# Kernel tuning notes

Measured on AMD Instinct MI355X. Metric: run time of the kernel, lower is better.

## Reference

```python
import math
import jax, jax.numpy as jnp
import numpy as np

S, B, H = 512, 64, 1024

def setup_inputs() -> dict:
    key = jax.random.key(0)
    ks = jax.random.split(key, 7)
    hidden = jax.random.normal(ks[0], (1, B, H), dtype=jnp.float32)
    encoder_outputs = jax.random.normal(ks[1], (S, B, H), dtype=jnp.float32)
    pe = jax.random.normal(ks[2], (B, S), dtype=jnp.float32)
    seq_mask = jax.random.bernoulli(ks[3], 0.1, (B, S))
    # nn.Linear(2H, H): weight (H, 2H), bias (H); nn.Linear(H, 1, bias=False): weight (1, H)
    Wa = jax.random.normal(ks[4], (H, 2 * H), dtype=jnp.float32) * (1.0 / math.sqrt(2 * H))
    ba = jax.random.normal(ks[5], (H,), dtype=jnp.float32) * 0.01
    Ws = jax.random.normal(ks[6], (1, H), dtype=jnp.float32) * (1.0 / math.sqrt(H))
    return {"hidden": hidden, "encoder_outputs": encoder_outputs, "pe": pe,
            "seq_mask": seq_mask, "Wa": Wa, "ba": ba, "Ws": Ws}

def reference(hidden, encoder_outputs, pe, seq_mask, Wa, ba, Ws):
    max_len, bsz, hdim = encoder_outputs.shape
    factor = 1.0 / math.sqrt(hdim)
    scale = factor * math.log(max_len)
    # repeat hidden along seq dim, concat on feature dim -> (S, B, 2H)
    h_rep = jnp.broadcast_to(hidden, (max_len, bsz, hdim))
    energy_in = jnp.concatenate([h_rep, encoder_outputs], axis=2)  # (S, B, 2H)
    e = jax.nn.relu(jnp.einsum('sbf,hf->sbh', energy_in, Wa) + ba)  # (S, B, H)
    attn = scale * jnp.einsum('sbh,oh->sbo', e, Ws)[..., 0]          # (S, B)
    attn = attn.T + pe                                               # (B, S)
    attn = jnp.where(seq_mask, jnp.float32(-1e12), attn)
    attn = jax.nn.softmax(attn, axis=1)
    return attn[:, None, :]  # (B, 1, S)
```

## Files before the change

### kernel.cpp

```cpp
#include <hip/hip_runtime.h>
#include <hip/hip_bf16.h>

#define S_LEN 512
#define BSZ 64
#define HDIM 1024
#define H2 2048

typedef float f32x4 __attribute__((ext_vector_type(4)));
typedef short short8 __attribute__((ext_vector_type(8)));
typedef __bf16 bf16x8 __attribute__((ext_vector_type(8)));

__device__ __forceinline__ unsigned short f2bf(float x) {
    union { float f; unsigned u; } v; v.f = x;
    unsigned r = (v.u + 0x7FFFu + ((v.u >> 16) & 1u)) >> 16;
    return (unsigned short)r;
}

__global__ __launch_bounds__(256) void k_zero(float* __restrict__ p) {
    p[blockIdx.x * 256 + threadIdx.x] = 0.f;
}

__global__ __launch_bounds__(256) void k_e1(const float* __restrict__ hidden,
                                            const float* __restrict__ Wa,
                                            const float* __restrict__ ba,
                                            float* __restrict__ e1) {
    __shared__ __align__(16) float hsh[HDIM];
    int b = blockIdx.x >> 2;
    int h = ((blockIdx.x & 3) << 8) + threadIdx.x;
    for (int i = threadIdx.x; i < HDIM; i += 256) hsh[i] = hidden[b * HDIM + i];
    __syncthreads();
    const float* wr = Wa + (size_t)h * H2;
    float acc = 0.f;
#pragma unroll 8
    for (int k = 0; k < HDIM; k += 4) {
        f32x4 w = *(const f32x4*)(wr + k);
        f32x4 hh = *(const f32x4*)(hsh + k);
        acc += w[0] * hh[0] + w[1] * hh[1] + w[2] * hh[2] + w[3] * hh[3];
    }
    e1[b * HDIM + h] = acc + ba[h];
}

__global__ __launch_bounds__(256) void k_packB(const float* __restrict__ Wa,
                                               unsigned short* __restrict__ wsB) {
    int ci = blockIdx.x * 256 + threadIdx.x;
    int tile = ci >> 9;
    int wi = ci & 511;
    int row = wi >> 2;
    int slot = wi & 3;
    int nt = tile >> 5, kt = tile & 31;
    int n = nt * 128 + row;
    int kk = kt * 32 + ((slot ^ ((row >> 1) & 3)) << 3);
    const float* src = Wa + (size_t)n * H2 + HDIM + kk;
    f32x4 a = *(const f32x4*)src;
    f32x4 b = *(const f32x4*)(src + 4);
    short8 o;
    o[0] = (short)f2bf(a[0]); o[1] = (short)f2bf(a[1]);
    o[2] = (short)f2bf(a[2]); o[3] = (short)f2bf(a[3]);
    o[4] = (short)f2bf(b[0]); o[5] = (short)f2bf(b[1]);
    o[6] = (short)f2bf(b[2]); o[7] = (short)f2bf(b[3]);
    *(short8*)(wsB + (size_t)ci * 8) = o;
}

__global__ __launch_bounds__(256) void k_main(const float* __restrict__ enc,
                                              const unsigned short* __restrict__ wsB,
                                              const float* __restrict__ e1,
                                              const float* __restrict__ Ws,
                                              float* __restrict__ logits) {
    __shared__ __align__(16) unsigned short As[4096];
    __shared__ __align__(16) unsigned short Bs[4096];

    int i = blockIdx.x;
    int mt = ((i >> 6) << 3) | (i & 7);
    int nt = (i >> 3) & 7;
    int r0 = mt * 128;
    int n0 = nt * 128;

    int tid = threadIdx.x;
    int lane = tid & 63, wid = tid >> 6;
    int wr = wid >> 1, wc = wid & 1;
    int c = lane & 15, g = lane >> 4;

    f32x4 acc[4][4] = {};

    for (int k0 = 0; k0 < HDIM; k0 += 32) {
        const unsigned short* bsrc = wsB + ((size_t)(nt * 32 + (k0 >> 5)) << 12);
        char* lbase = (char*)Bs + wid * 1024;
        __builtin_amdgcn_global_load_lds(
            (const __attribute__((address_space(1))) void*)(bsrc + (size_t)tid * 8),
            (__attribute__((address_space(3))) void*)lbase, 16, 0, 0);
        __builtin_amdgcn_global_load_lds(
            (const __attribute__((address_space(1))) void*)(bsrc + (size_t)(tid + 256) * 8),
            (__attribute__((address_space(3))) void*)(lbase + 4096), 16, 0, 0);

#pragma unroll
        for (int it = 0; it < 2; ++it) {
            int row = (it << 6) + (tid >> 2);
            int slot = tid & 3;
            int kk = k0 + ((slot ^ ((row >> 1) & 3)) << 3);
            const float* src = enc + (size_t)(r0 + row) * HDIM + kk;
            f32x4 a = *(const f32x4*)src;
            f32x4 b = *(const f32x4*)(src + 4);
            short8 o;
            o[0] = (short)f2bf(a[0]); o[1] = (short)f2bf(a[1]);
            o[2] = (short)f2bf(a[2]); o[3] = (short)f2bf(a[3]);
            o[4] = (short)f2bf(b[0]); o[5] = (short)f2bf(b[1]);
            o[6] = (short)f2bf(b[2]); o[7] = (short)f2bf(b[3]);
            *(short8*)((char*)As + row * 64 + slot * 16) = o;
        }
        __syncthreads();

        bf16x8 af[4], bfr[4];
#pragma unroll
        for (int m = 0; m < 4; ++m) {
            int row = wr * 64 + m * 16 + c;
            int slot = g ^ ((row >> 1) & 3);
            af[m] = *(const bf16x8*)((const char*)As + row * 64 + slot * 16);
        }
#pragma unroll
        for (int n = 0; n < 4; ++n) {
            int rowb = wc * 64 + n * 16 + c;
            int slot = g ^ ((rowb >> 1) & 3);
            bfr[n] = *(const bf16x8*)((const char*)Bs + rowb * 64 + slot * 16);
        }
#pragma unroll
        for (int m = 0; m < 4; ++m)
#pragma unroll
            for (int n = 0; n < 4; ++n)
                acc[m][n] = __builtin_amdgcn_mfma_f32_16x16x32_bf16(af[m], bfr[n], acc[m][n], 0, 0, 0);
        __syncthreads();
    }

    float wsv[4];
#pragma unroll
    for (int n = 0; n < 4; ++n) wsv[n] = Ws[n0 + wc * 64 + n * 16 + c];

#pragma unroll
    for (int m = 0; m < 4; ++m) {
#pragma unroll
        for (int j = 0; j < 4; ++j) {
            int rl = wr * 64 + m * 16 + g * 4 + j;
            int r = r0 + rl;
            int b = r & 63, sidx = r >> 6;
            const float* e1b = e1 + b * HDIM + n0 + wc * 64;
            float p = 0.f;
#pragma unroll
            for (int n = 0; n < 4; ++n) {
                float v = acc[m][n][j] + e1b[n * 16 + c];
                v = fmaxf(v, 0.f);
                p += v * wsv[n];
            }
            p += __shfl_xor(p, 1);
            p += __shfl_xor(p, 2);
            p += __shfl_xor(p, 4);
            p += __shfl_xor(p, 8);
            if (c == 0) atomicAdd(&logits[b * S_LEN + sidx], p);
        }
    }
}

__global__ __launch_bounds__(512) void k_softmax(float* __restrict__ out,
                                                 const float* __restrict__ pe,
                                                 const int* __restrict__ mask,
                                                 float scale) {
    __shared__ float red[8];
    int b = blockIdx.x, s = threadIdx.x;
    int idx = (b << 9) + s;
    float acc = out[idx];
    float logit = (mask[idx] != 0) ? -1e12f : (scale * acc + pe[idx]);
    float m = logit;
#pragma unroll
    for (int o = 32; o >= 1; o >>= 1) m = fmaxf(m, __shfl_xor(m, o));
    if ((s & 63) == 0) red[s >> 6] = m;
    __syncthreads();
    float m2 = red[0];
#pragma unroll
    for (int i2 = 1; i2 < 8; ++i2) m2 = fmaxf(m2, red[i2]);
    float e = expf(logit - m2);
    float t = e;
#pragma unroll
    for (int o = 32; o >= 1; o >>= 1) t += __shfl_xor(t, o);
    __syncthreads();
    if ((s & 63) == 0) red[s >> 6] = t;
    __syncthreads();
    float tot = 0.f;
#pragma unroll
    for (int i2 = 0; i2 < 8; ++i2) tot += red[i2];
    out[idx] = e / tot;
}

extern "C" void kernel_launch(void* const* d_in, const int* in_sizes, int n_in,
                              void* d_out, int out_size, void* d_ws, size_t ws_size,
                              hipStream_t stream) {
    const float* hidden = (const float*)d_in[0];
    const float* enc    = (const float*)d_in[1];
    const float* pe     = (const float*)d_in[2];
    const int*   mask   = (const int*)d_in[3];
    const float* Wa     = (const float*)d_in[4];
    const float* ba     = (const float*)d_in[5];
    const float* Ws     = (const float*)d_in[6];
    float* out = (float*)d_out;

    float* e1 = (float*)d_ws;
    unsigned short* wsB = (unsigned short*)((char*)d_ws + 262144);

    const float scale = 0.19494764453248462f;

    k_zero<<<128, 256, 0, stream>>>(out);
    k_e1<<<256, 256, 0, stream>>>(hidden, Wa, ba, e1);
    k_packB<<<512, 256, 0, stream>>>(Wa, wsB);
    k_main<<<2048, 256, 0, stream>>>(enc, wsB, e1, Ws, out);
    k_softmax<<<64, 512, 0, stream>>>(out, pe, mask, scale);
}
```

Before: 393.3 us.

## Pre-pack encoder outputs to bf16 tiles and load both GEMM operands via LDS DMA

Adds a separate pass that converts the fp32 encoder outputs into swizzled bf16 tiles, so the main GEMM can stream both A and B directly into LDS with global_load_lds instead of converting fp32 in every block. The aim is to stop each N-tile block from re-reading and re-converting fp32 A eight times. The cost is an extra kernel and 64MB of workspace traffic, and the fallback path is used when the workspace is too small. k_e1 is also rewritten to use one wavefront per output with a shuffle reduction, and bf16 conversion now uses native casts.

```diff
diff --git a/kernel.cpp b/kernel.cpp
--- a/kernel.cpp
+++ b/kernel.cpp
@@ -10,12 +10,6 @@
 typedef short short8 __attribute__((ext_vector_type(8)));
 typedef __bf16 bf16x8 __attribute__((ext_vector_type(8)));
 
-__device__ __forceinline__ unsigned short f2bf(float x) {
-    union { float f; unsigned u; } v; v.f = x;
-    unsigned r = (v.u + 0x7FFFu + ((v.u >> 16) & 1u)) >> 16;
-    return (unsigned short)r;
-}
-
 __global__ __launch_bounds__(256) void k_zero(float* __restrict__ p) {
     p[blockIdx.x * 256 + threadIdx.x] = 0.f;
 }
@@ -24,20 +18,21 @@
                                             const float* __restrict__ Wa,
                                             const float* __restrict__ ba,
                                             float* __restrict__ e1) {
-    __shared__ __align__(16) float hsh[HDIM];
-    int b = blockIdx.x >> 2;
-    int h = ((blockIdx.x & 3) << 8) + threadIdx.x;
-    for (int i = threadIdx.x; i < HDIM; i += 256) hsh[i] = hidden[b * HDIM + i];
-    __syncthreads();
+    int wg = blockIdx.x * 4 + (threadIdx.x >> 6);
+    int lane = threadIdx.x & 63;
+    int b = wg >> 10, h = wg & 1023;
+    const float* hr = hidden + b * HDIM;
     const float* wr = Wa + (size_t)h * H2;
     float acc = 0.f;
-#pragma unroll 8
-    for (int k = 0; k < HDIM; k += 4) {
-        f32x4 w = *(const f32x4*)(wr + k);
-        f32x4 hh = *(const f32x4*)(hsh + k);
-        acc += w[0] * hh[0] + w[1] * hh[1] + w[2] * hh[2] + w[3] * hh[3];
-    }
-    e1[b * HDIM + h] = acc + ba[h];
+#pragma unroll
+    for (int j = 0; j < 4; ++j) {
+        f32x4 hv = *(const f32x4*)(hr + j * 256 + lane * 4);
+        f32x4 wv = *(const f32x4*)(wr + j * 256 + lane * 4);
+        acc += hv[0] * wv[0] + hv[1] * wv[1] + hv[2] * wv[2] + hv[3] * wv[3];
+    }
+#pragma unroll
+    for (int o = 32; o >= 1; o >>= 1) acc += __shfl_xor(acc, o);
+    if (lane == 0) e1[wg] = acc + ba[h];
 }
 
 __global__ __launch_bounds__(256) void k_packB(const float* __restrict__ Wa,
@@ -53,19 +48,35 @@
     const float* src = Wa + (size_t)n * H2 + HDIM + kk;
     f32x4 a = *(const f32x4*)src;
     f32x4 b = *(const f32x4*)(src + 4);
-    short8 o;
-    o[0] = (short)f2bf(a[0]); o[1] = (short)f2bf(a[1]);
-    o[2] = (short)f2bf(a[2]); o[3] = (short)f2bf(a[3]);
-    o[4] = (short)f2bf(b[0]); o[5] = (short)f2bf(b[1]);
-    o[6] = (short)f2bf(b[2]); o[7] = (short)f2bf(b[3]);
-    *(short8*)(wsB + (size_t)ci * 8) = o;
-}
-
-__global__ __launch_bounds__(256) void k_main(const float* __restrict__ enc,
-                                              const unsigned short* __restrict__ wsB,
-                                              const float* __restrict__ e1,
-                                              const float* __restrict__ Ws,
-                                              float* __restrict__ logits) {
+    bf16x8 o;
+    o[0] = (__bf16)a[0]; o[1] = (__bf16)a[1]; o[2] = (__bf16)a[2]; o[3] = (__bf16)a[3];
+    o[4] = (__bf16)b[0]; o[5] = (__bf16)b[1]; o[6] = (__bf16)b[2]; o[7] = (__bf16)b[3];
+    *(bf16x8*)(wsB + (size_t)ci * 8) = o;
+}
+
+__global__ __launch_bounds__(256) void k_packA(const float* __restrict__ enc,
+                                               unsigned short* __restrict__ wsA) {
+    int ci = blockIdx.x * 256 + threadIdx.x;
+    const float* src = enc + (size_t)ci * 8;
+    f32x4 a = *(const f32x4*)src;
+    f32x4 b = *(const f32x4*)(src + 4);
+    int row_g = ci >> 7;
+    int cchunk = ci & 127;
+    int kt = cchunk >> 2, slot_src = cchunk & 3;
+    int mt = row_g >> 7, row = row_g & 127;
+    int slot = slot_src ^ ((row >> 1) & 3);
+    size_t dst = ((((size_t)(mt * 32 + kt)) << 9) + (row << 2) + slot) << 3;
+    bf16x8 o;
+    o[0] = (__bf16)a[0]; o[1] = (__bf16)a[1]; o[2] = (__bf16)a[2]; o[3] = (__bf16)a[3];
+    o[4] = (__bf16)b[0]; o[5] = (__bf16)b[1]; o[6] = (__bf16)b[2]; o[7] = (__bf16)b[3];
+    *(bf16x8*)(wsA + dst) = o;
+}
+
+__global__ __launch_bounds__(256) void k_main_pre(const unsigned short* __restrict__ wsA,
+                                                  const unsigned short* __restrict__ wsB,
+                                                  const float* __restrict__ e1,
+                                                  const float* __restrict__ Ws,
+                                                  float* __restrict__ logits) {
     __shared__ __align__(16) unsigned short As[4096];
     __shared__ __align__(16) unsigned short Bs[4096];
 
@@ -83,14 +94,104 @@
     f32x4 acc[4][4] = {};
 
     for (int k0 = 0; k0 < HDIM; k0 += 32) {
+        int kt = k0 >> 5;
+        const unsigned short* asrc = wsA + ((size_t)(mt * 32 + kt) << 12);
+        const unsigned short* bsrc = wsB + ((size_t)(nt * 32 + kt) << 12);
+        char* la = (char*)As + wid * 1024;
+        char* lb = (char*)Bs + wid * 1024;
+        __builtin_amdgcn_global_load_lds(
+            (const __attribute__((address_space(1))) void*)(asrc + (size_t)tid * 8),
+            (__attribute__((address_space(3))) void*)la, 16, 0, 0);
+        __builtin_amdgcn_global_load_lds(
+            (const __attribute__((address_space(1))) void*)(asrc + (size_t)(tid + 256) * 8),
+            (__attribute__((address_space(3))) void*)(la + 4096), 16, 0, 0);
+        __builtin_amdgcn_global_load_lds(
+            (const __attribute__((address_space(1))) void*)(bsrc + (size_t)tid * 8),
+            (__attribute__((address_space(3))) void*)lb, 16, 0, 0);
+        __builtin_amdgcn_global_load_lds(
+            (const __attribute__((address_space(1))) void*)(bsrc + (size_t)(tid + 256) * 8),
+            (__attribute__((address_space(3))) void*)(lb + 4096), 16, 0, 0);
+        __syncthreads();
+
+        bf16x8 af[4], bfr[4];
+#pragma unroll
+        for (int m = 0; m < 4; ++m) {
+            int row = wr * 64 + m * 16 + c;
+            int slot = g ^ ((row >> 1) & 3);
+            af[m] = *(const bf16x8*)((const char*)As + row * 64 + slot * 16);
+        }
+#pragma unroll
+        for (int n = 0; n < 4; ++n) {
+            int rowb = wc * 64 + n * 16 + c;
+            int slot = g ^ ((rowb >> 1) & 3);
+            bfr[n] = *(const bf16x8*)((const char*)Bs + rowb * 64 + slot * 16);
+        }
+#pragma unroll
+        for (int m = 0; m < 4; ++m)
+#pragma unroll
+            for (int n = 0; n < 4; ++n)
+                acc[m][n] = __builtin_amdgcn_mfma_f32_16x16x32_bf16(af[m], bfr[n], acc[m][n], 0, 0, 0);
+        __syncthreads();
+    }
+
+    float wsv[4];
+#pragma unroll
+    for (int n = 0; n < 4; ++n) wsv[n] = Ws[n0 + wc * 64 + n * 16 + c];
+
+#pragma unroll
+    for (int m = 0; m < 4; ++m) {
+#pragma unroll
+        for (int j = 0; j < 4; ++j) {
+            int rl = wr * 64 + m * 16 + g * 4 + j;
+            int r = r0 + rl;
+            int b = r & 63, sidx = r >> 6;
+            const float* e1b = e1 + b * HDIM + n0 + wc * 64;
+            float p = 0.f;
+#pragma unroll
+            for (int n = 0; n < 4; ++n) {
+                float v = acc[m][n][j] + e1b[n * 16 + c];
+                v = fmaxf(v, 0.f);
+                p += v * wsv[n];
+            }
+            p += __shfl_xor(p, 1);
+            p += __shfl_xor(p, 2);
+            p += __shfl_xor(p, 4);
+            p += __shfl_xor(p, 8);
+            if (c == 0) atomicAdd(&logits[b * S_LEN + sidx], p);
+        }
+    }
+}
+
+__global__ __launch_bounds__(256) void k_main_cvt(const float* __restrict__ enc,
+                                                  const unsigned short* __restrict__ wsB,
+                                                  const float* __restrict__ e1,
+                                                  const float* __restrict__ Ws,
+                                                  float* __restrict__ logits) {
+    __shared__ __align__(16) unsigned short As[4096];
+    __shared__ __align__(16) unsigned short Bs[4096];
+
+    int i = blockIdx.x;
+    int mt = ((i >> 6) << 3) | (i & 7);
+    int nt = (i >> 3) & 7;
+    int r0 = mt * 128;
+    int n0 = nt * 128;
+
+    int tid = threadIdx.x;
+    int lane = tid & 63, wid = tid >> 6;
+    int wr = wid >> 1, wc = wid & 1;
+    int c = lane & 15, g = lane >> 4;
+
+    f32x4 acc[4][4] = {};
+
+    for (int k0 = 0; k0 < HDIM; k0 += 32) {
         const unsigned short* bsrc = wsB + ((size_t)(nt * 32 + (k0 >> 5)) << 12);
-        char* lbase = (char*)Bs + wid * 1024;
+        char* lb = (char*)Bs + wid * 1024;
         __builtin_amdgcn_global_load_lds(
             (const __attribute__((address_space(1))) void*)(bsrc + (size_t)tid * 8),
-            (__attribute__((address_space(3))) void*)lbase, 16, 0, 0);
+            (__attribute__((address_space(3))) void*)lb, 16, 0, 0);
         __builtin_amdgcn_global_load_lds(
             (const __attribute__((address_space(1))) void*)(bsrc + (size_t)(tid + 256) * 8),
-            (__attribute__((address_space(3))) void*)(lbase + 4096), 16, 0, 0);
+            (__attribute__((address_space(3))) void*)(lb + 4096), 16, 0, 0);
 
 #pragma unroll
         for (int it = 0; it < 2; ++it) {
@@ -100,12 +201,10 @@
             const float* src = enc + (size_t)(r0 + row) * HDIM + kk;
             f32x4 a = *(const f32x4*)src;
             f32x4 b = *(const f32x4*)(src + 4);
-            short8 o;
-            o[0] = (short)f2bf(a[0]); o[1] = (short)f2bf(a[1]);
-            o[2] = (short)f2bf(a[2]); o[3] = (short)f2bf(a[3]);
-            o[4] = (short)f2bf(b[0]); o[5] = (short)f2bf(b[1]);
-            o[6] = (short)f2bf(b[2]); o[7] = (short)f2bf(b[3]);
-            *(short8*)((char*)As + row * 64 + slot * 16) = o;
+            bf16x8 o;
+            o[0] = (__bf16)a[0]; o[1] = (__bf16)a[1]; o[2] = (__bf16)a[2]; o[3] = (__bf16)a[3];
+            o[4] = (__bf16)b[0]; o[5] = (__bf16)b[1]; o[6] = (__bf16)b[2]; o[7] = (__bf16)b[3];
+            *(bf16x8*)((char*)As + row * 64 + slot * 16) = o;
         }
         __syncthreads();
 
@@ -202,12 +301,21 @@
 
     float* e1 = (float*)d_ws;
     unsigned short* wsB = (unsigned short*)((char*)d_ws + 262144);
+    unsigned short* wsA = (unsigned short*)((char*)d_ws + 262144 + 2097152);
+
+    const size_t need = 262144 + 2097152 + (size_t)32768 * 1024 * 2;
+    const bool pre = ws_size >= need;
 
     const float scale = 0.19494764453248462f;
 
     k_zero<<<128, 256, 0, stream>>>(out);
-    k_e1<<<256, 256, 0, stream>>>(hidden, Wa, ba, e1);
+    k_e1<<<16384, 256, 0, stream>>>(hidden, Wa, ba, e1);
     k_packB<<<512, 256, 0, stream>>>(Wa, wsB);
-    k_main<<<2048, 256, 0, stream>>>(enc, wsB, e1, Ws, out);
+    if (pre) {
+        k_packA<<<16384, 256, 0, stream>>>(enc, wsA);
+        k_main_pre<<<2048, 256, 0, stream>>>(wsA, wsB, e1, Ws, out);
+    } else {
+        k_main_cvt<<<2048, 256, 0, stream>>>(enc, wsB, e1, Ws, out);
+    }
     k_softmax<<<64, 512, 0, stream>>>(out, pe, mask, scale);
 }
```

Result: faster. 370.5 us (-5.8%).
